# Performance work log

Measured on AMD Instinct MI355X. Metric: run time of the kernel, lower is better.

## Reference

```python
import jax, jax.numpy as jnp
import numpy as np

FORGET_BIAS = 1.0  # TF LSTMCell default

def _lstm_step(c, h, x, W, b):
    # TF BasicLSTM/LSTMCell gate order: i, j (cell candidate), f, o
    z = jnp.concatenate([x, h], axis=-1) @ W + b
    i, j, f, o = jnp.split(z, 4, axis=-1)
    c_new = c * jax.nn.sigmoid(f + FORGET_BIAS) + jax.nn.sigmoid(i) * jnp.tanh(j)
    h_new = jnp.tanh(c_new) * jax.nn.sigmoid(o)
    return c_new, h_new

def setup_inputs() -> dict:
    key = jax.random.key(0)
    k1, k2, k3 = jax.random.split(key, 3)
    B, T, D, H1, H2 = 512, 2048, 1, 64, 1
    x = jax.random.normal(k1, (B, T, D), dtype=jnp.float32)
    W1 = jax.random.normal(k2, (D + H1, 4 * H1), dtype=jnp.float32) * 0.1
    b1 = jnp.zeros((4 * H1,), dtype=jnp.float32)
    W2 = jax.random.normal(k3, (H1 + H2, 4 * H2), dtype=jnp.float32) * 0.1
    b2 = jnp.zeros((4 * H2,), dtype=jnp.float32)
    return {"x": x, "W1": W1, "b1": b1, "W2": W2, "b2": b2}

def reference(x, W1, b1, W2, b2):
    B = x.shape[0]
    H1 = W1.shape[1] // 4
    H2 = W2.shape[1] // 4
    init = (jnp.zeros((B, H1), x.dtype), jnp.zeros((B, H1), x.dtype),
            jnp.zeros((B, H2), x.dtype), jnp.zeros((B, H2), x.dtype))

    def step(carry, x_t):
        c1, h1, c2, h2 = carry
        c1, h1 = _lstm_step(c1, h1, x_t, W1, b1)   # layer 1: LSTMCell(64)
        c2, h2 = _lstm_step(c2, h2, h1, W2, b2)    # layer 2: LSTMCell(1)
        return (c1, h1, c2, h2), h2

    xs = jnp.swapaxes(x, 0, 1)           # [T, B, 1]
    _, ys = jax.lax.scan(step, init, xs)  # ys: [T, B, 1]
    return jnp.swapaxes(ys, 0, 1)         # [B, T, 1]
```

## Files before the change

kernel.cpp:

```cpp
#include <hip/hip_runtime.h>

#define TT 2048

typedef float v2f __attribute__((ext_vector_type(2)));
typedef _Float16 h2v __attribute__((ext_vector_type(2)));

__device__ __forceinline__ v2f mk2(float a, float b) { v2f r; r.x = a; r.y = b; return r; }
__device__ __forceinline__ float rcpf(float x) { return __builtin_amdgcn_rcpf(x); }
__device__ __forceinline__ float fsig(float x) { return rcpf(1.0f + __expf(-x)); }
__device__ __forceinline__ float ftanh(float x) {
    return fmaf(2.0f, rcpf(1.0f + __expf(-2.0f * x)), -1.0f);
}

template<int C>
__device__ __forceinline__ float dppmov(float s) {
    return __int_as_float(__builtin_amdgcn_update_dpp(
        __float_as_int(s), __float_as_int(s), C, 0xF, 0xF, false));
}
template<int Q>
__device__ __forceinline__ float qbcast(float x) {
    return __int_as_float(__builtin_amdgcn_update_dpp(
        __float_as_int(x), __float_as_int(x), Q * 0x55, 0xF, 0xF, false));
}

#if __has_builtin(__builtin_amdgcn_fdot2)
#define DOT2(a, b, c) __builtin_amdgcn_fdot2((a), (b), (c), false)
#else
#define DOT2(a, b, c) fmaf((float)(a).x, (float)(b).x, \
                      fmaf((float)(a).y, (float)(b).y, (c)))
#endif

__device__ __forceinline__ h2v pk2(float a, float b) {
#if __has_builtin(__builtin_amdgcn_cvt_pkrtz)
    return __builtin_bit_cast(h2v, __builtin_amdgcn_cvt_pkrtz(a, b));
#else
    h2v r; r.x = (_Float16)a; r.y = (_Float16)b; return r;
#endif
}
__device__ __forceinline__ h2v bch(int v) { return __builtin_bit_cast(h2v, v); }

__global__ __launch_bounds__(64)
__attribute__((amdgpu_waves_per_eu(2, 2)))
void lstm1_f16(const float* __restrict__ x,
               const float* __restrict__ W1,
               const float* __restrict__ b1,
               const float* __restrict__ W2,
               float* __restrict__ zout)
{
    __shared__ __align__(16) float xall[TT];
    __shared__ __align__(16) _Float16 hring[16 * 72];

    const int lane = threadIdx.x & 63;
    const int e    = blockIdx.x;
    const int u    = lane;

    for (int i = lane; i < TT; i += 64) xall[i] = x[(size_t)e * TT + i];
    for (int i = lane; i < 576; i += 64) ((int*)hring)[i] = 0;

#define DWQ(G, GO, q) \
    const h2v w##G##q##x = pk2(W1[(1+8*(q))*256 + (GO)*64 + u], W1[(2+8*(q))*256 + (GO)*64 + u]); \
    const h2v w##G##q##y = pk2(W1[(3+8*(q))*256 + (GO)*64 + u], W1[(4+8*(q))*256 + (GO)*64 + u]); \
    const h2v w##G##q##z = pk2(W1[(5+8*(q))*256 + (GO)*64 + u], W1[(6+8*(q))*256 + (GO)*64 + u]); \
    const h2v w##G##q##w = pk2(W1[(7+8*(q))*256 + (GO)*64 + u], W1[(8+8*(q))*256 + (GO)*64 + u]);
    DWQ(I, 0, 0) DWQ(I, 0, 1) DWQ(I, 0, 2) DWQ(I, 0, 3)
    DWQ(I, 0, 4) DWQ(I, 0, 5) DWQ(I, 0, 6) DWQ(I, 0, 7)
    DWQ(J, 1, 0) DWQ(J, 1, 1) DWQ(J, 1, 2) DWQ(J, 1, 3)
    DWQ(J, 1, 4) DWQ(J, 1, 5) DWQ(J, 1, 6) DWQ(J, 1, 7)
    DWQ(F, 2, 0) DWQ(F, 2, 1) DWQ(F, 2, 2) DWQ(F, 2, 3)
    DWQ(F, 2, 4) DWQ(F, 2, 5) DWQ(F, 2, 6) DWQ(F, 2, 7)
    DWQ(O, 3, 0) DWQ(O, 3, 1) DWQ(O, 3, 2) DWQ(O, 3, 3)
    DWQ(O, 3, 4) DWQ(O, 3, 5) DWQ(O, 3, 6) DWQ(O, 3, 7)
#undef DWQ

    const float w0I = W1[u],        bI = b1[u];
    const float w0J = W1[64 + u],   bJ = b1[64 + u];
    const float w0F = W1[128 + u],  bF = b1[128 + u] + 1.0f;
    const float w0O = W1[192 + u],  bO = b1[192 + u];

    const int tl = lane >> 2, gq = lane & 3;
#define DW2(q) \
    const h2v w2##q##x = pk2(W2[(8*(q)+0)*4 + gq], W2[(8*(q)+1)*4 + gq]); \
    const h2v w2##q##y = pk2(W2[(8*(q)+2)*4 + gq], W2[(8*(q)+3)*4 + gq]); \
    const h2v w2##q##z = pk2(W2[(8*(q)+4)*4 + gq], W2[(8*(q)+5)*4 + gq]); \
    const h2v w2##q##w = pk2(W2[(8*(q)+6)*4 + gq], W2[(8*(q)+7)*4 + gq]);
    DW2(0) DW2(1) DW2(2) DW2(3) DW2(4) DW2(5) DW2(6) DW2(7)
#undef DW2

    float c1 = 0.0f;
    __syncthreads();

    float* __restrict__ zb = zout + (size_t)e * TT * 4;

#define DGQ(G, q, v) \
    acc##G = DOT2(bch((v).x), w##G##q##x, acc##G); \
    acc##G = DOT2(bch((v).y), w##G##q##y, acc##G); \
    acc##G = DOT2(bch((v).z), w##G##q##z, acc##G); \
    acc##G = DOT2(bch((v).w), w##G##q##w, acc##G);

    for (int t = 0; t < TT; ++t) {
        const int4* hp = (const int4*)&hring[((t - 1) & 15) * 72];
        const int4 q0 = hp[0], q1 = hp[1], q2 = hp[2], q3 = hp[3];
        const int4 q4 = hp[4], q5 = hp[5], q6 = hp[6], q7 = hp[7];
        const float xt = xall[t];
        float accI = fmaf(xt, w0I, bI);
        float accJ = fmaf(xt, w0J, bJ);
        float accF = fmaf(xt, w0F, bF);
        float accO = fmaf(xt, w0O, bO);
        DGQ(I, 0, q0) DGQ(J, 0, q0) DGQ(F, 0, q0) DGQ(O, 0, q0)
        DGQ(I, 1, q1) DGQ(J, 1, q1) DGQ(F, 1, q1) DGQ(O, 1, q1)
        DGQ(I, 2, q2) DGQ(J, 2, q2) DGQ(F, 2, q2) DGQ(O, 2, q2)
        DGQ(I, 3, q3) DGQ(J, 3, q3) DGQ(F, 3, q3) DGQ(O, 3, q3)
        DGQ(I, 4, q4) DGQ(J, 4, q4) DGQ(F, 4, q4) DGQ(O, 4, q4)
        DGQ(I, 5, q5) DGQ(J, 5, q5) DGQ(F, 5, q5) DGQ(O, 5, q5)
        DGQ(I, 6, q6) DGQ(J, 6, q6) DGQ(F, 6, q6) DGQ(O, 6, q6)
        DGQ(I, 7, q7) DGQ(J, 7, q7) DGQ(F, 7, q7) DGQ(O, 7, q7)
        const float i_ = fsig(accI);
        const float j_ = ftanh(accJ);
        const float f_ = fsig(accF);
        const float o_ = fsig(accO);
        c1 = fmaf(c1, f_, i_ * j_);
        const float h1 = ftanh(c1) * o_;
        hring[(t & 15) * 72 + u] = (_Float16)h1;

        if ((t & 15) == 15) {
            const int4* hb = (const int4*)&hring[tl * 72];
            const int4 b0 = hb[0], b1q = hb[1], b2q = hb[2], b3 = hb[3];
            const int4 b4 = hb[4], b5 = hb[5], b6 = hb[6], b7 = hb[7];
            float z2 = 0.0f;
#define BQ(q, v) \
            z2 = DOT2(bch((v).x), w2##q##x, z2); \
            z2 = DOT2(bch((v).y), w2##q##y, z2); \
            z2 = DOT2(bch((v).z), w2##q##z, z2); \
            z2 = DOT2(bch((v).w), w2##q##w, z2);
            BQ(0, b0) BQ(1, b1q) BQ(2, b2q) BQ(3, b3)
            BQ(4, b4) BQ(5, b5) BQ(6, b6) BQ(7, b7)
#undef BQ
            zb[(size_t)(t - 15 + tl) * 4 + gq] = z2;
        }
    }
#undef DGQ
}

__global__ __launch_bounds__(64)
void lstm2_chain(const float* __restrict__ zp,
                 const float* __restrict__ W2,
                 const float* __restrict__ b2,
                 float* __restrict__ out)
{
    const int lane = threadIdx.x & 63;
    const int e    = lane >> 2;
    const int g    = lane & 3;
    const int elem = (blockIdx.x << 4) + e;

    const float w2h = W2[256 + g];
    const float bb  = b2[g] + ((g == 2) ? 1.0f : 0.0f);
    const float nlm = (g == 1) ? -2.0f : -1.0f;
    const float k2  = (g == 1) ?  2.0f :  1.0f;
    const float k3  = (g == 1) ? -1.0f :  0.0f;

    const float* __restrict__ zrow = zp + (size_t)elem * TT * 4 + g;
    float* __restrict__ orow = out + (size_t)elem * TT;

    float c2 = 0.0f, h2 = 0.0f;

    float zc[16];
#pragma unroll
    for (int k = 0; k < 16; ++k) zc[k] = zrow[k << 2];

    for (int t0 = 0; t0 < TT; t0 += 16) {
        float zn[16];
        if (t0 + 16 < TT) {
#pragma unroll
            for (int k = 0; k < 16; ++k) zn[k] = zrow[((t0 + 16 + k) << 2)];
        }
        float st0 = 0.f, st1 = 0.f, st2 = 0.f, st3 = 0.f;
#pragma unroll
        for (int k = 0; k < 16; ++k) {
            const float arg = fmaf(w2h, h2, zc[k] + bb);
            const float ev  = __expf(arg * nlm);
            const float rv  = rcpf(1.0f + ev);
            const float v   = fmaf(k2, rv, k3);
            const float vi = qbcast<0>(v), vj = qbcast<1>(v);
            const float vf = qbcast<2>(v), vo = qbcast<3>(v);
            c2 = fmaf(c2, vf, vi * vj);
            h2 = ftanh(c2) * vo;
            const bool mine = (g == (k & 3));
            if ((k >> 2) == 0) st0 = mine ? h2 : st0;
            else if ((k >> 2) == 1) st1 = mine ? h2 : st1;
            else if ((k >> 2) == 2) st2 = mine ? h2 : st2;
            else st3 = mine ? h2 : st3;
        }
        orow[t0 + g]      = st0;
        orow[t0 + 4 + g]  = st1;
        orow[t0 + 8 + g]  = st2;
        orow[t0 + 12 + g] = st3;
#pragma unroll
        for (int k = 0; k < 16; ++k) zc[k] = zn[k];
    }
}

__global__ __launch_bounds__(512)
__attribute__((amdgpu_waves_per_eu(4, 4)))
void lstm2_mono(const float* __restrict__ x,
                const float* __restrict__ W1,
                const float* __restrict__ b1,
                const float* __restrict__ W2,
                const float* __restrict__ b2,
                float* __restrict__ out)
{
    __shared__ __align__(16) float xall[TT + 4];
    __shared__ __align__(16) float h1x[2][80];
    __shared__ __align__(16) float zpq[4][4];
    __shared__ __align__(16) float h2buf[2][64];

    const int tid  = threadIdx.x;
    const int wave = tid >> 6;
    const int lane = tid & 63;
    const int b    = blockIdx.x;

    for (int i = tid; i < TT; i += 512) xall[i] = x[b * TT + i];
    if (tid < 4) xall[TT + tid] = 0.0f;

    const int u    = lane >> 3;
    const int h    = (lane >> 2) & 1;
    const int g    = lane & 3;
    const int unit = (wave << 3) + u;
    const int col  = (g << 6) + unit;

#define DECLW(k) const v2f wq##k = mk2(W1[(1 + 32*h + 2*(k)) * 256 + col], \
                                       W1[(2 + 32*h + 2*(k)) * 256 + col]);
    DECLW(0)  DECLW(1)  DECLW(2)  DECLW(3)
    DECLW(4)  DECLW(5)  DECLW(6)  DECLW(7)
    DECLW(8)  DECLW(9)  DECLW(10) DECLW(11)
    DECLW(12) DECLW(13) DECLW(14) DECLW(15)
#undef DECLW

    const float w0x   = (h == 0) ? W1[col] : 0.0f;
    const float biasF = (h == 0) ? (b1[col] + ((g == 2) ? 1.0f : 0.0f)) : 0.0f;
    const float nlm   = (g == 1) ? -2.0f : -1.0f;
    const bool  isj   = (g == 1);

    const float w2g  = W2[lane * 4 + (wave & 3)];
    const float w2h0 = W2[256], w2h1 = W2[257], w2h2 = W2[258], w2h3 = W2[259];
    const float b20 = b2[0], b21 = b2[1], b22 = b2[2], b23 = b2[3];

    float c1 = 0.0f;
    float c2 = 0.0f, h2v2 = 0.0f;

    const int hbase = h * 48;
    const int ridx  = lane + ((lane >> 5) << 4);
    const int widx  = (unit < 32) ? unit : unit + 16;

    if (tid < 160) ((float*)h1x)[tid] = 0.0f;
    __syncthreads();

    float* __restrict__ outb = out + b * TT;

#define WSUM(s) ({ float _s = (s);                                            \
    _s += dppmov<0x111>(_s); _s += dppmov<0x112>(_s); _s += dppmov<0x114>(_s);\
    _s += dppmov<0x118>(_s); _s += dppmov<0x142>(_s); _s += dppmov<0x143>(_s);\
    _s; })

#define STEP(P, t, xv)                                                        \
    {                                                                         \
        if ((t) < TT) {                                                       \
            const float4* hp = (const float4*)&h1x[P][hbase];                 \
            const float4 q0 = hp[0], q1 = hp[1], q2 = hp[2], q3 = hp[3];      \
            const float4 q4 = hp[4], q5 = hp[5], q6 = hp[6], q7 = hp[7];      \
            v2f a0 = mk2(fmaf((xv), w0x, biasF), 0.0f);                       \
            v2f a1 = mk2(0.f, 0.f), a2 = mk2(0.f, 0.f), a3 = mk2(0.f, 0.f);  \
            a0 = __builtin_elementwise_fma(mk2(q0.x, q0.y), wq0,  a0);        \
            a1 = __builtin_elementwise_fma(mk2(q0.z, q0.w), wq1,  a1);        \
            a2 = __builtin_elementwise_fma(mk2(q1.x, q1.y), wq2,  a2);        \
            a3 = __builtin_elementwise_fma(mk2(q1.z, q1.w), wq3,  a3);        \
            a0 = __builtin_elementwise_fma(mk2(q2.x, q2.y), wq4,  a0);        \
            a1 = __builtin_elementwise_fma(mk2(q2.z, q2.w), wq5,  a1);        \
            a2 = __builtin_elementwise_fma(mk2(q3.x, q3.y), wq6,  a2);        \
            a3 = __builtin_elementwise_fma(mk2(q3.z, q3.w), wq7,  a3);        \
            a0 = __builtin_elementwise_fma(mk2(q4.x, q4.y), wq8,  a0);        \
            a1 = __builtin_elementwise_fma(mk2(q4.z, q4.w), wq9,  a1);        \
            a2 = __builtin_elementwise_fma(mk2(q5.x, q5.y), wq10, a2);        \
            a3 = __builtin_elementwise_fma(mk2(q5.z, q5.w), wq11, a3);        \
            a0 = __builtin_elementwise_fma(mk2(q6.x, q6.y), wq12, a0);        \
            a1 = __builtin_elementwise_fma(mk2(q6.z, q6.w), wq13, a1);        \
            a2 = __builtin_elementwise_fma(mk2(q7.x, q7.y), wq14, a2);        \
            a3 = __builtin_elementwise_fma(mk2(q7.z, q7.w), wq15, a3);        \
            const v2f sv = (a0 + a1) + (a2 + a3);                             \
            const float zh = sv.x + sv.y;                                     \
            const float tshr = dppmov<0x114>(zh);                             \
            const float tshl = dppmov<0x104>(zh);                             \
            const float zfull = zh + (h ? tshr : tshl);                       \
            const float e = __expf(zfull * nlm);                              \
            const float r = rcpf(1.0f + e);                                   \
            const float v = isj ? fmaf(2.0f, r, -1.0f) : r;                   \
            const float gi = qbcast<0>(v), gj = qbcast<1>(v);                 \
            const float gf = qbcast<2>(v), go = qbcast<3>(v);                 \
            c1 = fmaf(c1, gf, gi * gj);                                       \
            const float h1v = ftanh(c1) * go;                                 \
            if ((lane & 7) == 0) h1x[(P) ^ 1][widx] = h1v;                    \
        }                                                                     \
        if (wave < 4 && (t) >= 1 && (t) <= TT) {                              \
            const float s = WSUM(h1x[P][ridx] * w2g);                         \
            if (lane == 63) zpq[((t) - 1) & 3][wave] = s;                     \
        }                                                                     \
        if (wave == 7 && lane == 0 && (t) >= 2 && (t) <= TT + 1) {            \
            const int st = (t) - 2;                                           \
            const float4 z4 = *(const float4*)zpq[st & 3];                    \
            const float zi = z4.x + fmaf(h2v2, w2h0, b20);                    \
            const float zj = z4.y + fmaf(h2v2, w2h1, b21);                    \
            const float zf = z4.z + fmaf(h2v2, w2h2, b22);                    \
            const float zo = z4.w + fmaf(h2v2, w2h3, b23);                    \
            c2 = c2 * fsig(zf + 1.0f) + fsig(zi) * ftanh(zj);                 \
            h2v2 = ftanh(c2) * fsig(zo);                                      \
            h2buf[(st >> 6) & 1][st & 63] = h2v2;                             \
        }                                                                     \
        __syncthreads();                                                      \
        if (wave == 4 && (t) >= 66 && ((t) & 63) == 2) {                      \
            const int blk = ((t) - 66) >> 6;                                  \
            outb[(blk << 6) + lane] = h2buf[blk & 1][lane];                   \
        }                                                                     \
    }

    for (int it = 0; it <= TT + 2; it += 2) {
        const float2 x2 = *(const float2*)&xall[it];
        STEP(0, it,     x2.x)
        STEP(1, it + 1, x2.y)
    }
#undef STEP
#undef WSUM
}

extern "C" void kernel_launch(void* const* d_in, const int* in_sizes, int n_in,
                              void* d_out, int out_size, void* d_ws, size_t ws_size,
                              hipStream_t stream)
{
    const float* x  = (const float*)d_in[0];
    const float* W1 = (const float*)d_in[1];
    const float* b1 = (const float*)d_in[2];
    const float* W2 = (const float*)d_in[3];
    const float* b2 = (const float*)d_in[4];
    float* out = (float*)d_out;

    const size_t need = (size_t)512 * TT * 4 * sizeof(float);
    if (ws_size >= need) {
        float* zp = (float*)d_ws;
        lstm1_f16<<<512, 64, 0, stream>>>(x, W1, b1, W2, zp);
        lstm2_chain<<<512 / 16, 64, 0, stream>>>(zp, W2, b2, out);
    } else {
        lstm2_mono<<<512, 512, 0, stream>>>(x, W1, b1, W2, b2, out);
    }
}
```

Measured before the change: 1.039 ms.

## Process two batch elements per wavefront in layer-1 LSTM kernel

```diff
diff --git a/kernel.cpp b/kernel.cpp
--- a/kernel.cpp
+++ b/kernel.cpp
@@ -40,22 +40,27 @@
 __device__ __forceinline__ h2v bch(int v) { return __builtin_bit_cast(h2v, v); }
 
 __global__ __launch_bounds__(64)
-__attribute__((amdgpu_waves_per_eu(2, 2)))
-void lstm1_f16(const float* __restrict__ x,
-               const float* __restrict__ W1,
-               const float* __restrict__ b1,
-               const float* __restrict__ W2,
-               float* __restrict__ zout)
+__attribute__((amdgpu_waves_per_eu(1, 1)))
+void lstm1_f16x2(const float* __restrict__ x,
+                 const float* __restrict__ W1,
+                 const float* __restrict__ b1,
+                 const float* __restrict__ W2,
+                 float* __restrict__ zout)
 {
-    __shared__ __align__(16) float xall[TT];
-    __shared__ __align__(16) _Float16 hring[16 * 72];
+    __shared__ __align__(16) float xA[TT], xB[TT];
+    __shared__ __align__(16) _Float16 ringA[16 * 72], ringB[16 * 72];
 
     const int lane = threadIdx.x & 63;
     const int e    = blockIdx.x;
     const int u    = lane;
 
-    for (int i = lane; i < TT; i += 64) xall[i] = x[(size_t)e * TT + i];
-    for (int i = lane; i < 576; i += 64) ((int*)hring)[i] = 0;
+    for (int i = lane; i < TT; i += 64) {
+        xA[i] = x[(size_t)(2 * e) * TT + i];
+        xB[i] = x[(size_t)(2 * e + 1) * TT + i];
+    }
+    for (int i = lane; i < 576; i += 64) {
+        ((int*)ringA)[i] = 0; ((int*)ringB)[i] = 0;
+    }
 
 #define DWQ(G, GO, q) \
     const h2v w##G##q##x = pk2(W1[(1+8*(q))*256 + (GO)*64 + u], W1[(2+8*(q))*256 + (GO)*64 + u]); \
@@ -86,59 +91,88 @@
     DW2(0) DW2(1) DW2(2) DW2(3) DW2(4) DW2(5) DW2(6) DW2(7)
 #undef DW2
 
-    float c1 = 0.0f;
+    float c1A = 0.0f, c1B = 0.0f;
     __syncthreads();
 
-    float* __restrict__ zb = zout + (size_t)e * TT * 4;
-
-#define DGQ(G, q, v) \
-    acc##G = DOT2(bch((v).x), w##G##q##x, acc##G); \
-    acc##G = DOT2(bch((v).y), w##G##q##y, acc##G); \
-    acc##G = DOT2(bch((v).z), w##G##q##z, acc##G); \
-    acc##G = DOT2(bch((v).w), w##G##q##w, acc##G);
+    float* __restrict__ zbA = zout + (size_t)(2 * e) * TT * 4;
+    float* __restrict__ zbB = zout + (size_t)(2 * e + 1) * TT * 4;
+
+#define DOTQ(E, q, v) \
+    accI##E = DOT2(bch((v).x), wI##q##x, accI##E); \
+    accI##E = DOT2(bch((v).y), wI##q##y, accI##E); \
+    accI##E = DOT2(bch((v).z), wI##q##z, accI##E); \
+    accI##E = DOT2(bch((v).w), wI##q##w, accI##E); \
+    accJ##E = DOT2(bch((v).x), wJ##q##x, accJ##E); \
+    accJ##E = DOT2(bch((v).y), wJ##q##y, accJ##E); \
+    accJ##E = DOT2(bch((v).z), wJ##q##z, accJ##E); \
+    accJ##E = DOT2(bch((v).w), wJ##q##w, accJ##E); \
+    accF##E = DOT2(bch((v).x), wF##q##x, accF##E); \
+    accF##E = DOT2(bch((v).y), wF##q##y, accF##E); \
+    accF##E = DOT2(bch((v).z), wF##q##z, accF##E); \
+    accF##E = DOT2(bch((v).w), wF##q##w, accF##E); \
+    accO##E = DOT2(bch((v).x), wO##q##x, accO##E); \
+    accO##E = DOT2(bch((v).y), wO##q##y, accO##E); \
+    accO##E = DOT2(bch((v).z), wO##q##z, accO##E); \
+    accO##E = DOT2(bch((v).w), wO##q##w, accO##E);
 
     for (int t = 0; t < TT; ++t) {
-        const int4* hp = (const int4*)&hring[((t - 1) & 15) * 72];
-        const int4 q0 = hp[0], q1 = hp[1], q2 = hp[2], q3 = hp[3];
-        const int4 q4 = hp[4], q5 = hp[5], q6 = hp[6], q7 = hp[7];
-        const float xt = xall[t];
-        float accI = fmaf(xt, w0I, bI);
-        float accJ = fmaf(xt, w0J, bJ);
-        float accF = fmaf(xt, w0F, bF);
-        float accO = fmaf(xt, w0O, bO);
-        DGQ(I, 0, q0) DGQ(J, 0, q0) DGQ(F, 0, q0) DGQ(O, 0, q0)
-        DGQ(I, 1, q1) DGQ(J, 1, q1) DGQ(F, 1, q1) DGQ(O, 1, q1)
-        DGQ(I, 2, q2) DGQ(J, 2, q2) DGQ(F, 2, q2) DGQ(O, 2, q2)
-        DGQ(I, 3, q3) DGQ(J, 3, q3) DGQ(F, 3, q3) DGQ(O, 3, q3)
-        DGQ(I, 4, q4) DGQ(J, 4, q4) DGQ(F, 4, q4) DGQ(O, 4, q4)
-        DGQ(I, 5, q5) DGQ(J, 5, q5) DGQ(F, 5, q5) DGQ(O, 5, q5)
-        DGQ(I, 6, q6) DGQ(J, 6, q6) DGQ(F, 6, q6) DGQ(O, 6, q6)
-        DGQ(I, 7, q7) DGQ(J, 7, q7) DGQ(F, 7, q7) DGQ(O, 7, q7)
-        const float i_ = fsig(accI);
-        const float j_ = ftanh(accJ);
-        const float f_ = fsig(accF);
-        const float o_ = fsig(accO);
-        c1 = fmaf(c1, f_, i_ * j_);
-        const float h1 = ftanh(c1) * o_;
-        hring[(t & 15) * 72 + u] = (_Float16)h1;
+        const int rs = ((t - 1) & 15) * 72;
+        const int4* hpA = (const int4*)&ringA[rs];
+        const int4* hpB = (const int4*)&ringB[rs];
+        const int4 a0 = hpA[0], a1 = hpA[1], a2 = hpA[2], a3 = hpA[3];
+        const int4 b0 = hpB[0], b1q = hpB[1], b2q = hpB[2], b3q = hpB[3];
+        const int4 a4 = hpA[4], a5 = hpA[5], a6 = hpA[6], a7 = hpA[7];
+        const int4 b4 = hpB[4], b5 = hpB[5], b6 = hpB[6], b7 = hpB[7];
+        const float xtA = xA[t], xtB = xB[t];
+        float accIA = fmaf(xtA, w0I, bI), accIB = fmaf(xtB, w0I, bI);
+        float accJA = fmaf(xtA, w0J, bJ), accJB = fmaf(xtB, w0J, bJ);
+        float accFA = fmaf(xtA, w0F, bF), accFB = fmaf(xtB, w0F, bF);
+        float accOA = fmaf(xtA, w0O, bO), accOB = fmaf(xtB, w0O, bO);
+        DOTQ(A, 0, a0) DOTQ(B, 0, b0)
+        DOTQ(A, 1, a1) DOTQ(B, 1, b1q)
+        DOTQ(A, 2, a2) DOTQ(B, 2, b2q)
+        DOTQ(A, 3, a3) DOTQ(B, 3, b3q)
+        DOTQ(A, 4, a4) DOTQ(B, 4, b4)
+        DOTQ(A, 5, a5) DOTQ(B, 5, b5)
+        DOTQ(A, 6, a6) DOTQ(B, 6, b6)
+        DOTQ(A, 7, a7) DOTQ(B, 7, b7)
+        const float iA = fsig(accIA),  iB = fsig(accIB);
+        const float jA = ftanh(accJA), jB = ftanh(accJB);
+        const float fA = fsig(accFA),  fB = fsig(accFB);
+        const float oA = fsig(accOA),  oB = fsig(accOB);
+        c1A = fmaf(c1A, fA, iA * jA);
+        c1B = fmaf(c1B, fB, iB * jB);
+        const float h1A = ftanh(c1A) * oA;
+        const float h1B = ftanh(c1B) * oB;
+        const int ws = (t & 15) * 72 + u;
+        ringA[ws] = (_Float16)h1A;
+        ringB[ws] = (_Float16)h1B;
 
         if ((t & 15) == 15) {
-            const int4* hb = (const int4*)&hring[tl * 72];
-            const int4 b0 = hb[0], b1q = hb[1], b2q = hb[2], b3 = hb[3];
-            const int4 b4 = hb[4], b5 = hb[5], b6 = hb[6], b7 = hb[7];
-            float z2 = 0.0f;
-#define BQ(q, v) \
-            z2 = DOT2(bch((v).x), w2##q##x, z2); \
-            z2 = DOT2(bch((v).y), w2##q##y, z2); \
-            z2 = DOT2(bch((v).z), w2##q##z, z2); \
-            z2 = DOT2(bch((v).w), w2##q##w, z2);
-            BQ(0, b0) BQ(1, b1q) BQ(2, b2q) BQ(3, b3)
-            BQ(4, b4) BQ(5, b5) BQ(6, b6) BQ(7, b7)
+            const int4* hbA = (const int4*)&ringA[tl * 72];
+            const int4* hbB = (const int4*)&ringB[tl * 72];
+            float zA = 0.0f, zB = 0.0f;
+#define BQ(q, E, hb) \
+            { const int4 v = (hb)[q]; \
+              z##E = DOT2(bch(v.x), w2##q##x, z##E); \
+              z##E = DOT2(bch(v.y), w2##q##y, z##E); \
+              z##E = DOT2(bch(v.z), w2##q##z, z##E); \
+              z##E = DOT2(bch(v.w), w2##q##w, z##E); }
+            BQ(0, A, hbA) BQ(0, B, hbB)
+            BQ(1, A, hbA) BQ(1, B, hbB)
+            BQ(2, A, hbA) BQ(2, B, hbB)
+            BQ(3, A, hbA) BQ(3, B, hbB)
+            BQ(4, A, hbA) BQ(4, B, hbB)
+            BQ(5, A, hbA) BQ(5, B, hbB)
+            BQ(6, A, hbA) BQ(6, B, hbB)
+            BQ(7, A, hbA) BQ(7, B, hbB)
 #undef BQ
-            zb[(size_t)(t - 15 + tl) * 4 + gq] = z2;
+            const size_t zoff = (size_t)(t - 15 + tl) * 4 + gq;
+            zbA[zoff] = zA;
+            zbB[zoff] = zB;
         }
     }
-#undef DGQ
+#undef DOTQ
 }
 
 __global__ __launch_bounds__(64)
@@ -344,7 +378,7 @@
     const size_t need = (size_t)512 * TT * 4 * sizeof(float);
     if (ws_size >= need) {
         float* zp = (float*)d_ws;
-        lstm1_f16<<<512, 64, 0, stream>>>(x, W1, b1, W2, zp);
+        lstm1_f16x2<<<256, 64, 0, stream>>>(x, W1, b1, W2, zp);
         lstm2_chain<<<512 / 16, 64, 0, stream>>>(zp, W2, b2, out);
     } else {
         lstm2_mono<<<512, 512, 0, stream>>>(x, W1, b1, W2, b2, out);
```

After: 1.669 ms. 1.61x slower.
